# Optimization experiments

Measured on AMD Instinct MI355X. Metric: run time of the kernel, lower is better.

The kernel has to match this reference:

```python
import jax, jax.numpy as jnp
import numpy as np

N_NODES = 50000
N_EDGES = 800000
N_GRAPHS = 2000
F = 256          # node feature dim == hidden_dim (required by stacked convs)
HID = 256
L = 4
FP = 1034
BN_EPS = 1e-5


def setup_inputs() -> dict:
    key = jax.random.key(0)
    ks = jax.random.split(key, 20)
    s = 0.05
    x = jax.random.normal(ks[0], (N_NODES, F), dtype=jnp.float32)
    edge_index = jax.random.randint(ks[1], (2, N_EDGES), 0, N_NODES, dtype=jnp.int64)
    edge_attr = jax.random.normal(ks[2], (N_EDGES, 1), dtype=jnp.float32)
    fingerprint = jax.random.uniform(ks[3], (N_GRAPHS, FP), dtype=jnp.float32)
    batch = jnp.sort(jax.random.randint(ks[4], (N_NODES,), 0, N_GRAPHS, dtype=jnp.int64))
    # stacked per-layer conv params: message linear [(F+1)->HID], update linear [HID->HID]
    lin_w = jax.random.normal(ks[5], (L, F + 1, HID), dtype=jnp.float32) * s
    lin_b = jax.random.normal(ks[6], (L, HID), dtype=jnp.float32) * s
    upd_w = jax.random.normal(ks[7], (L, HID, HID), dtype=jnp.float32) * s
    upd_b = jax.random.normal(ks[8], (L, HID), dtype=jnp.float32) * s
    # gated-attention pooling gate_nn: Linear(HID,HID) -> tanh -> Linear(HID,1)
    g1_w = jax.random.normal(ks[9], (HID, HID), dtype=jnp.float32) * s
    g1_b = jax.random.normal(ks[10], (HID,), dtype=jnp.float32) * s
    g2_w = jax.random.normal(ks[11], (HID, 1), dtype=jnp.float32) * s
    g2_b = jax.random.normal(ks[12], (1,), dtype=jnp.float32) * s
    fc1_w = jax.random.normal(ks[13], (HID + FP, HID), dtype=jnp.float32) * s
    fc1_b = jax.random.normal(ks[14], (HID,), dtype=jnp.float32) * s
    bn_gamma = jnp.ones((HID,), dtype=jnp.float32)
    bn_beta = jnp.zeros((HID,), dtype=jnp.float32)
    fc2_w = jax.random.normal(ks[15], (HID, 1), dtype=jnp.float32) * s
    fc2_b = jax.random.normal(ks[16], (1,), dtype=jnp.float32) * s
    return dict(x=x, edge_index=edge_index, edge_attr=edge_attr,
                fingerprint=fingerprint, batch=batch,
                lin_w=lin_w, lin_b=lin_b, upd_w=upd_w, upd_b=upd_b,
                g1_w=g1_w, g1_b=g1_b, g2_w=g2_w, g2_b=g2_b,
                fc1_w=fc1_w, fc1_b=fc1_b, bn_gamma=bn_gamma, bn_beta=bn_beta,
                fc2_w=fc2_w, fc2_b=fc2_b)


def reference(x, edge_index, edge_attr, fingerprint, batch,
              lin_w, lin_b, upd_w, upd_b,
              g1_w, g1_b, g2_w, g2_b,
              fc1_w, fc1_b, bn_gamma, bn_beta, fc2_w, fc2_b):
    n = x.shape[0]
    b = fingerprint.shape[0]
    loop = jnp.arange(n, dtype=edge_index.dtype)
    src = jnp.concatenate([edge_index[0], loop])   # x_j = source nodes (PyG default)
    dst = jnp.concatenate([edge_index[1], loop])   # aggregate at target
    ea = jnp.concatenate([edge_attr, jnp.zeros((n, edge_attr.shape[1]), edge_attr.dtype)], axis=0)
    for l in range(L):
        wn, we = lin_w[l, :F], lin_w[l, F:]        # split concat([x_j, edge_attr]) @ W
        msg = jax.nn.relu(x[src] @ wn + ea @ we + lin_b[l])          # [E+n, HID]
        aggr = jax.ops.segment_sum(msg, dst, num_segments=n)          # scatter-add
        x = jax.nn.relu(aggr @ upd_w[l] + upd_b[l])
    # gated attention pooling
    gate = jax.nn.sigmoid(jnp.tanh(x @ g1_w + g1_b) @ g2_w + g2_b)    # [n, 1]
    pooled = jax.ops.segment_sum(x * gate, batch, num_segments=b)     # [b, HID]
    h = jnp.concatenate([pooled, fingerprint], axis=1) @ fc1_w + fc1_b
    # BatchNorm1d (training mode: biased batch stats)
    mu = jnp.mean(h, axis=0)
    var = jnp.mean((h - mu) ** 2, axis=0)
    h = (h - mu) * jax.lax.rsqrt(var + BN_EPS) * bn_gamma + bn_beta
    h = jax.nn.relu(h)  # dropout is identity in eval mode
    return (h @ fc2_w + fc2_b).squeeze(-1)        # [b]
```

## Files before the change

### kernel.cpp

```cpp
#include <hip/hip_runtime.h>
#include <math.h>

#define HIDF 256
#define FPDIM 1034
#define MPAD 50048
#define FCM 2048
#define FCK 1344

typedef _Float16 f16x8 __attribute__((ext_vector_type(8)));
typedef _Float16 f16x4 __attribute__((ext_vector_type(4)));
typedef float f32x4 __attribute__((ext_vector_type(4)));

__device__ __forceinline__ float relu_f(float v) { return fmaxf(v, 0.f); }

__global__ __launch_bounds__(256) void convxh_k(
    const float* __restrict__ x, _Float16* __restrict__ xh, int n)
{
    int i = blockIdx.x * 256 + threadIdx.x;
    int row = i >> 6;
    if (row >= MPAD) return;
    f16x4 o;
    if (row < n) {
        float4 v = ((const float4*)x)[i];
        o[0] = (_Float16)v.x; o[1] = (_Float16)v.y;
        o[2] = (_Float16)v.z; o[3] = (_Float16)v.w;
    } else {
        o[0] = o[1] = o[2] = o[3] = (_Float16)0.f;
    }
    ((f16x4*)xh)[i] = o;
}

__global__ __launch_bounds__(256) void convw_k(
    const float* __restrict__ w, _Float16* __restrict__ whi,
    _Float16* __restrict__ wlo)
{
    int i = blockIdx.x * 256 + threadIdx.x;
    int nn = i >> 8, kk = i & 255;
    float v = w[kk * 256 + nn];
    _Float16 h = (_Float16)v;
    _Float16 l = (_Float16)(v - (float)h);
    whi[i] = h;
    wlo[i] = l;
}

__global__ __launch_bounds__(256) void convfc1a_k(
    const float* __restrict__ pooled, const float* __restrict__ fp,
    _Float16* __restrict__ ahi, _Float16* __restrict__ alo, int B)
{
    int i = blockIdx.x * 256 + threadIdx.x;
    if (i >= FCM * FCK) return;
    int row = i / FCK, col = i - row * FCK;
    float v = 0.f;
    if (row < B) {
        if (col < HIDF) v = pooled[(size_t)row * HIDF + col];
        else if (col < HIDF + FPDIM) v = fp[(size_t)row * FPDIM + (col - HIDF)];
    }
    _Float16 h = (_Float16)v;
    _Float16 l = (_Float16)(v - (float)h);
    ahi[i] = h;
    alo[i] = l;
}

__global__ __launch_bounds__(256) void convfc1w_k(
    const float* __restrict__ w, _Float16* __restrict__ whi,
    _Float16* __restrict__ wlo)
{
    int i = blockIdx.x * 256 + threadIdx.x;
    if (i >= HIDF * FCK) return;
    int nn = i / FCK, kk = i - nn * FCK;
    float v = (kk < HIDF + FPDIM) ? w[(size_t)kk * HIDF + nn] : 0.f;
    _Float16 h = (_Float16)v;
    _Float16 l = (_Float16)(v - (float)h);
    whi[i] = h;
    wlo[i] = l;
}

template <int ACT>
__global__ __launch_bounds__(256) void gemm_f16(
    const _Float16* __restrict__ A, const _Float16* __restrict__ Whi,
    const _Float16* __restrict__ Wlo, const float* __restrict__ bias,
    _Float16* __restrict__ C, int M, int N, int K)
{
    __shared__ _Float16 As[128 * 64];
    __shared__ _Float16 Bh[128 * 64];
    __shared__ _Float16 Bl[128 * 64];
    const int tid = threadIdx.x;
    const int wave = tid >> 6, lane = tid & 63;
    const int m0 = blockIdx.y * 128, n0 = blockIdx.x * 128;
    const int wr = wave >> 1, wc = wave & 1;

    f32x4 acc[4][4];
#pragma unroll
    for (int i = 0; i < 4; ++i)
#pragma unroll
        for (int j = 0; j < 4; ++j) acc[i][j] = (f32x4){0.f, 0.f, 0.f, 0.f};

    const int lrow = lane >> 3;
    const int lcol8 = (lane & 7) * 8;

    for (int k0 = 0; k0 < K; k0 += 64) {
#pragma unroll
        for (int i = 0; i < 4; ++i) {
            int iss = wave * 4 + i;
            int row = 8 * iss + lrow;
            const _Float16* ga = A   + (size_t)(m0 + row) * K + k0 + lcol8;
            const _Float16* gh = Whi + (size_t)(n0 + row) * K + k0 + lcol8;
            const _Float16* gl = Wlo + (size_t)(n0 + row) * K + k0 + lcol8;
            __builtin_amdgcn_global_load_lds(
                (const __attribute__((address_space(1))) void*)ga,
                (__attribute__((address_space(3))) void*)(As + iss * 512), 16, 0, 0);
            __builtin_amdgcn_global_load_lds(
                (const __attribute__((address_space(1))) void*)gh,
                (__attribute__((address_space(3))) void*)(Bh + iss * 512), 16, 0, 0);
            __builtin_amdgcn_global_load_lds(
                (const __attribute__((address_space(1))) void*)gl,
                (__attribute__((address_space(3))) void*)(Bl + iss * 512), 16, 0, 0);
        }
        __syncthreads();
#pragma unroll
        for (int kk = 0; kk < 2; ++kk) {
            const int kb = kk * 32 + (lane >> 4) * 8;
            f16x8 af[4], bh[4], bl[4];
#pragma unroll
            for (int mi = 0; mi < 4; ++mi)
                af[mi] = *(const f16x8*)&As[(wr * 64 + mi * 16 + (lane & 15)) * 64 + kb];
#pragma unroll
            for (int ni = 0; ni < 4; ++ni) {
                int r = (wc * 64 + ni * 16 + (lane & 15)) * 64 + kb;
                bh[ni] = *(const f16x8*)&Bh[r];
                bl[ni] = *(const f16x8*)&Bl[r];
            }
#pragma unroll
            for (int mi = 0; mi < 4; ++mi)
#pragma unroll
                for (int ni = 0; ni < 4; ++ni) {
                    acc[mi][ni] = __builtin_amdgcn_mfma_f32_16x16x32_f16(
                        af[mi], bh[ni], acc[mi][ni], 0, 0, 0);
                    acc[mi][ni] = __builtin_amdgcn_mfma_f32_16x16x32_f16(
                        af[mi], bl[ni], acc[mi][ni], 0, 0, 0);
                }
        }
        __syncthreads();
    }

    const int crow0 = m0 + wr * 64 + (lane >> 4) * 4;
    const int ccol0 = n0 + wc * 64 + (lane & 15);
#pragma unroll
    for (int mi = 0; mi < 4; ++mi) {
#pragma unroll
        for (int ni = 0; ni < 4; ++ni) {
            int col = ccol0 + ni * 16;
            float bv = bias ? bias[col] : 0.f;
#pragma unroll
            for (int r = 0; r < 4; ++r) {
                int row = crow0 + mi * 16 + r;
                float v = acc[mi][ni][r] + bv;
                if (ACT == 1) v = relu_f(v);
                else if (ACT == 2) v = tanhf(v);
                C[(size_t)row * N + col] = (_Float16)v;
            }
        }
    }
}

__global__ __launch_bounds__(256) void gemm_fc1(
    const _Float16* __restrict__ Ahi, const _Float16* __restrict__ Alo,
    const _Float16* __restrict__ Whi, const _Float16* __restrict__ Wlo,
    const float* __restrict__ bias, float* __restrict__ C,
    int Mv, int N, int K)
{
    __shared__ _Float16 Ah[128 * 64];
    __shared__ _Float16 Al[128 * 64];
    __shared__ _Float16 Bh[128 * 64];
    __shared__ _Float16 Bl[128 * 64];
    const int tid = threadIdx.x;
    const int wave = tid >> 6, lane = tid & 63;
    const int m0 = blockIdx.y * 128, n0 = blockIdx.x * 128;
    const int wr = wave >> 1, wc = wave & 1;

    f32x4 acc[4][4];
#pragma unroll
    for (int i = 0; i < 4; ++i)
#pragma unroll
        for (int j = 0; j < 4; ++j) acc[i][j] = (f32x4){0.f, 0.f, 0.f, 0.f};

    const int lrow = lane >> 3;
    const int lcol8 = (lane & 7) * 8;

    for (int k0 = 0; k0 < K; k0 += 64) {
#pragma unroll
        for (int i = 0; i < 4; ++i) {
            int iss = wave * 4 + i;
            int row = 8 * iss + lrow;
            const _Float16* gah = Ahi + (size_t)(m0 + row) * K + k0 + lcol8;
            const _Float16* gal = Alo + (size_t)(m0 + row) * K + k0 + lcol8;
            const _Float16* gbh = Whi + (size_t)(n0 + row) * K + k0 + lcol8;
            const _Float16* gbl = Wlo + (size_t)(n0 + row) * K + k0 + lcol8;
            __builtin_amdgcn_global_load_lds(
                (const __attribute__((address_space(1))) void*)gah,
                (__attribute__((address_space(3))) void*)(Ah + iss * 512), 16, 0, 0);
            __builtin_amdgcn_global_load_lds(
                (const __attribute__((address_space(1))) void*)gal,
                (__attribute__((address_space(3))) void*)(Al + iss * 512), 16, 0, 0);
            __builtin_amdgcn_global_load_lds(
                (const __attribute__((address_space(1))) void*)gbh,
                (__attribute__((address_space(3))) void*)(Bh + iss * 512), 16, 0, 0);
            __builtin_amdgcn_global_load_lds(
                (const __attribute__((address_space(1))) void*)gbl,
                (__attribute__((address_space(3))) void*)(Bl + iss * 512), 16, 0, 0);
        }
        __syncthreads();
#pragma unroll
        for (int kk = 0; kk < 2; ++kk) {
            const int kb = kk * 32 + (lane >> 4) * 8;
            f16x8 ah[4], al[4], bh[4], bl[4];
#pragma unroll
            for (int mi = 0; mi < 4; ++mi) {
                int r = (wr * 64 + mi * 16 + (lane & 15)) * 64 + kb;
                ah[mi] = *(const f16x8*)&Ah[r];
                al[mi] = *(const f16x8*)&Al[r];
            }
#pragma unroll
            for (int ni = 0; ni < 4; ++ni) {
                int r = (wc * 64 + ni * 16 + (lane & 15)) * 64 + kb;
                bh[ni] = *(const f16x8*)&Bh[r];
                bl[ni] = *(const f16x8*)&Bl[r];
            }
#pragma unroll
            for (int mi = 0; mi < 4; ++mi)
#pragma unroll
                for (int ni = 0; ni < 4; ++ni) {
                    acc[mi][ni] = __builtin_amdgcn_mfma_f32_16x16x32_f16(
                        ah[mi], bh[ni], acc[mi][ni], 0, 0, 0);
                    acc[mi][ni] = __builtin_amdgcn_mfma_f32_16x16x32_f16(
                        ah[mi], bl[ni], acc[mi][ni], 0, 0, 0);
                    acc[mi][ni] = __builtin_amdgcn_mfma_f32_16x16x32_f16(
                        al[mi], bh[ni], acc[mi][ni], 0, 0, 0);
                }
        }
        __syncthreads();
    }

    const int crow0 = m0 + wr * 64 + (lane >> 4) * 4;
    const int ccol0 = n0 + wc * 64 + (lane & 15);
#pragma unroll
    for (int mi = 0; mi < 4; ++mi) {
#pragma unroll
        for (int ni = 0; ni < 4; ++ni) {
            int col = ccol0 + ni * 16;
            float bv = bias[col];
#pragma unroll
            for (int r = 0; r < 4; ++r) {
                int row = crow0 + mi * 16 + r;
                if (row < Mv)
                    C[(size_t)row * N + col] = acc[mi][ni][r] + bv;
            }
        }
    }
}

__global__ void count_k(const int* __restrict__ dst, int* __restrict__ cnt, int E)
{
    int e = blockIdx.x * blockDim.x + threadIdx.x;
    if (e < E) atomicAdd(&cnt[dst[e]], 1);
}

__global__ __launch_bounds__(256) void scan1_k(
    const int* __restrict__ cnt, int* __restrict__ offs,
    int* __restrict__ bsum, int n)
{
    __shared__ int sh[256];
    int t = threadIdx.x, idx = blockIdx.x * 256 + t;
    int v = (idx < n) ? cnt[idx] : 0;
    sh[t] = v;
    __syncthreads();
    for (int o = 1; o < 256; o <<= 1) {
        int a = (t >= o) ? sh[t - o] : 0;
        __syncthreads();
        sh[t] += a;
        __syncthreads();
    }
    if (idx < n) offs[idx] = sh[t] - v;
    if (t == 255) bsum[blockIdx.x] = sh[255];
}

__global__ __launch_bounds__(256) void scan2_k(int* __restrict__ bsum, int nb)
{
    __shared__ int sh[256];
    int t = threadIdx.x;
    int v = (t < nb) ? bsum[t] : 0;
    sh[t] = v;
    __syncthreads();
    for (int o = 1; o < 256; o <<= 1) {
        int a = (t >= o) ? sh[t - o] : 0;
        __syncthreads();
        sh[t] += a;
        __syncthreads();
    }
    if (t < nb) bsum[t] = sh[t] - v;
}

__global__ __launch_bounds__(256) void scan3_k(
    int* __restrict__ offs, const int* __restrict__ bsum,
    int* __restrict__ cursor, int n, int E)
{
    int idx = blockIdx.x * 256 + threadIdx.x;
    if (idx < n) {
        int o = offs[idx] + bsum[blockIdx.x];
        offs[idx] = o;
        cursor[idx] = o;
    }
    if (idx == 0) offs[n] = E;
}

__global__ void scatter_k(const int* __restrict__ dst, const int* __restrict__ src,
                          const float* __restrict__ ea, int* __restrict__ cursor,
                          int* __restrict__ srcS, float* __restrict__ eaS, int E)
{
    int e = blockIdx.x * blockDim.x + threadIdx.x;
    if (e < E) {
        int p = atomicAdd(&cursor[dst[e]], 1);
        srcS[p] = src[e];
        eaS[p] = ea[e];
    }
}

__global__ void start_k(const int* __restrict__ batch, int* __restrict__ start,
                        int n, int B)
{
    int g = blockIdx.x * blockDim.x + threadIdx.x;
    if (g > B) return;
    int lo = 0, hi = n;
    while (lo < hi) {
        int mid = (lo + hi) >> 1;
        if (batch[mid] < g) lo = mid + 1; else hi = mid;
    }
    start[g] = lo;
}

__global__ __launch_bounds__(256) void aggregate_k(
    const _Float16* __restrict__ xw, const float* __restrict__ we,
    const int* __restrict__ srcS, const float* __restrict__ eaS,
    const int* __restrict__ offs, _Float16* __restrict__ out, int n)
{
    int w = (blockIdx.x * blockDim.x + threadIdx.x) >> 6;
    if (w >= n) return;
    int lane = threadIdx.x & 63;
    int f = lane << 2;
    float4 we4 = *(const float4*)(we + f);
    f16x4 xs = *(const f16x4*)(xw + (size_t)w * HIDF + f);
    float4 acc;
    acc.x = relu_f((float)xs[0]);
    acc.y = relu_f((float)xs[1]);
    acc.z = relu_f((float)xs[2]);
    acc.w = relu_f((float)xs[3]);
    int e0 = offs[w], e1 = offs[w + 1];
    int ii = e0;
    for (; ii + 8 <= e1; ii += 8) {
        int s[8]; float a[8]; f16x4 v[8];
#pragma unroll
        for (int j = 0; j < 8; ++j) { s[j] = srcS[ii + j]; a[j] = eaS[ii + j]; }
#pragma unroll
        for (int j = 0; j < 8; ++j)
            v[j] = *(const f16x4*)(xw + (size_t)s[j] * HIDF + f);
#pragma unroll
        for (int j = 0; j < 8; ++j) {
            acc.x += relu_f(fmaf(a[j], we4.x, (float)v[j][0]));
            acc.y += relu_f(fmaf(a[j], we4.y, (float)v[j][1]));
            acc.z += relu_f(fmaf(a[j], we4.z, (float)v[j][2]));
            acc.w += relu_f(fmaf(a[j], we4.w, (float)v[j][3]));
        }
    }
    if (ii + 4 <= e1) {
        int s[4]; float a[4]; f16x4 v[4];
#pragma unroll
        for (int j = 0; j < 4; ++j) { s[j] = srcS[ii + j]; a[j] = eaS[ii + j]; }
#pragma unroll
        for (int j = 0; j < 4; ++j)
            v[j] = *(const f16x4*)(xw + (size_t)s[j] * HIDF + f);
#pragma unroll
        for (int j = 0; j < 4; ++j) {
            acc.x += relu_f(fmaf(a[j], we4.x, (float)v[j][0]));
            acc.y += relu_f(fmaf(a[j], we4.y, (float)v[j][1]));
            acc.z += relu_f(fmaf(a[j], we4.z, (float)v[j][2]));
            acc.w += relu_f(fmaf(a[j], we4.w, (float)v[j][3]));
        }
        ii += 4;
    }
    for (; ii < e1; ++ii) {
        int s0 = srcS[ii];
        float a0 = eaS[ii];
        f16x4 v0 = *(const f16x4*)(xw + (size_t)s0 * HIDF + f);
        acc.x += relu_f(fmaf(a0, we4.x, (float)v0[0]));
        acc.y += relu_f(fmaf(a0, we4.y, (float)v0[1]));
        acc.z += relu_f(fmaf(a0, we4.z, (float)v0[2]));
        acc.w += relu_f(fmaf(a0, we4.w, (float)v0[3]));
    }
    f16x4 o;
    o[0] = (_Float16)acc.x; o[1] = (_Float16)acc.y;
    o[2] = (_Float16)acc.z; o[3] = (_Float16)acc.w;
    *(f16x4*)(out + (size_t)w * HIDF + f) = o;
}

__global__ __launch_bounds__(256) void gate_k(
    const _Float16* __restrict__ t, const float* __restrict__ g2w,
    const float* __restrict__ g2b, float* __restrict__ gate, int n)
{
    int w = (blockIdx.x * blockDim.x + threadIdx.x) >> 6;
    if (w >= n) return;
    int lane = threadIdx.x & 63;
    f16x4 tv = *(const f16x4*)(t + (size_t)w * HIDF + (lane << 2));
    float4 g = *(const float4*)(g2w + (lane << 2));
    float s = (float)tv[0] * g.x + (float)tv[1] * g.y
            + (float)tv[2] * g.z + (float)tv[3] * g.w;
    for (int o = 32; o; o >>= 1) s += __shfl_xor(s, o);
    if (lane == 0) gate[w] = 1.f / (1.f + expf(-(s + g2b[0])));
}

__global__ __launch_bounds__(256) void pool_k(
    const _Float16* __restrict__ x, const float* __restrict__ gate,
    const int* __restrict__ start, float* __restrict__ pooled, int B)
{
    int w = (blockIdx.x * blockDim.x + threadIdx.x) >> 6;
    if (w >= B) return;
    int lane = threadIdx.x & 63;
    int f = lane << 2;
    float4 acc = make_float4(0.f, 0.f, 0.f, 0.f);
    int i0 = start[w], i1 = start[w + 1];
    for (int i = i0; i < i1; ++i) {
        float gi = gate[i];
        f16x4 v = *(const f16x4*)(x + (size_t)i * HIDF + f);
        acc.x = fmaf(gi, (float)v[0], acc.x);
        acc.y = fmaf(gi, (float)v[1], acc.y);
        acc.z = fmaf(gi, (float)v[2], acc.z);
        acc.w = fmaf(gi, (float)v[3], acc.w);
    }
    *(float4*)(pooled + (size_t)w * HIDF + f) = acc;
}

__global__ __launch_bounds__(256) void bnstats_k(
    const float* __restrict__ h, float* __restrict__ mu,
    float* __restrict__ rs, int B)
{
    int j = blockIdx.x;
    int tid = threadIdx.x;
    float s = 0.f, s2 = 0.f;
    for (int g = tid; g < B; g += 256) {
        float v = h[(size_t)g * HIDF + j];
        s += v;
        s2 = fmaf(v, v, s2);
    }
    __shared__ float sh[256], sh2[256];
    sh[tid] = s; sh2[tid] = s2;
    __syncthreads();
    for (int o = 128; o; o >>= 1) {
        if (tid < o) { sh[tid] += sh[tid + o]; sh2[tid] += sh2[tid + o]; }
        __syncthreads();
    }
    if (tid == 0) {
        float m = sh[0] / (float)B;
        float var = sh2[0] / (float)B - m * m;
        if (var < 0.f) var = 0.f;
        mu[j] = m;
        rs[j] = rsqrtf(var + 1e-5f);
    }
}

__global__ __launch_bounds__(256) void final_k(
    const float* __restrict__ h, const float* __restrict__ mu,
    const float* __restrict__ rs, const float* __restrict__ gamma,
    const float* __restrict__ beta, const float* __restrict__ w2,
    const float* __restrict__ b2, float* __restrict__ out, int B)
{
    int g = blockIdx.x;
    int j = threadIdx.x;
    float v = h[(size_t)g * HIDF + j];
    v = (v - mu[j]) * rs[j] * gamma[j] + beta[j];
    v = relu_f(v);
    float term = v * w2[j];
    __shared__ float sh[256];
    sh[j] = term;
    __syncthreads();
    for (int o = 128; o; o >>= 1) {
        if (j < o) sh[j] += sh[j + o];
        __syncthreads();
    }
    if (j == 0) out[g] = sh[0] + b2[0];
}

extern "C" void kernel_launch(void* const* d_in, const int* in_sizes, int n_in,
                              void* d_out, int out_size, void* d_ws, size_t ws_size,
                              hipStream_t stream)
{
    const float* x      = (const float*)d_in[0];
    const int*   ei     = (const int*)d_in[1];
    const float* ea     = (const float*)d_in[2];
    const float* fp     = (const float*)d_in[3];
    const int*   batch  = (const int*)d_in[4];
    const float* lin_w  = (const float*)d_in[5];
    const float* lin_b  = (const float*)d_in[6];
    const float* upd_w  = (const float*)d_in[7];
    const float* upd_b  = (const float*)d_in[8];
    const float* g1w    = (const float*)d_in[9];
    const float* g1b    = (const float*)d_in[10];
    const float* g2w    = (const float*)d_in[11];
    const float* g2b    = (const float*)d_in[12];
    const float* fc1w   = (const float*)d_in[13];
    const float* fc1b   = (const float*)d_in[14];
    const float* gamma  = (const float*)d_in[15];
    const float* beta   = (const float*)d_in[16];
    const float* fc2w   = (const float*)d_in[17];
    const float* fc2b   = (const float*)d_in[18];
    float* out = (float*)d_out;

    const int n = in_sizes[0] / HIDF;
    const int E = in_sizes[1] / 2;
    const int B = in_sizes[3] / FPDIM;
    const int L = in_sizes[5] / (257 * 256);
    const int* srcArr = ei;
    const int* dstArr = ei + E;
    const int nb = (n + 255) / 256;

    char* w = (char*)d_ws;
    _Float16* xh   = (_Float16*)w;  w += (size_t)MPAD * HIDF * 2;
    _Float16* bufA = (_Float16*)w;  w += (size_t)MPAD * HIDF * 2;
    _Float16* bufB = (_Float16*)w;  w += (size_t)MPAD * HIDF * 2;
    _Float16* whi = (_Float16*)w;  w += (size_t)9 * 65536 * 2;
    _Float16* wlo = (_Float16*)w;  w += (size_t)9 * 65536 * 2;
    _Float16* fahi = (_Float16*)w; w += (size_t)FCM * FCK * 2;
    _Float16* falo = (_Float16*)w; w += (size_t)FCM * FCK * 2;
    _Float16* fwhi = (_Float16*)w; w += (size_t)HIDF * FCK * 2;
    _Float16* fwlo = (_Float16*)w; w += (size_t)HIDF * FCK * 2;
    int*   srcS   = (int*)w;    w += (size_t)E * 4;
    float* eaS    = (float*)w;  w += (size_t)E * 4;
    int*   offs   = (int*)w;    w += ((size_t)n + 4) * 4;
    int*   cursor = (int*)w;    w += ((size_t)n + 4) * 4;
    int*   cnt    = (int*)w;    w += (size_t)n * 4;
    int*   bsum   = (int*)w;    w += 256 * 4;
    int*   startA = (int*)w;    w += ((size_t)B + 4) * 4;
    float* gateA  = (float*)w;  w += (size_t)n * 4;
    float* pooled = (float*)w;  w += (size_t)B * HIDF * 4;
    float* h      = (float*)w;  w += (size_t)B * HIDF * 4;
    float* mu     = (float*)w;  w += 256 * 4;
    float* rs     = (float*)w;  w += 256 * 4;

    hipMemsetAsync(cnt, 0, (size_t)n * 4, stream);
    count_k<<<(E + 255) / 256, 256, 0, stream>>>(dstArr, cnt, E);
    scan1_k<<<nb, 256, 0, stream>>>(cnt, offs, bsum, n);
    scan2_k<<<1, 256, 0, stream>>>(bsum, nb);
    scan3_k<<<nb, 256, 0, stream>>>(offs, bsum, cursor, n, E);
    scatter_k<<<(E + 255) / 256, 256, 0, stream>>>(dstArr, srcArr, ea, cursor, srcS, eaS, E);
    start_k<<<(B + 256) / 256, 256, 0, stream>>>(batch, startA, n, B);

    convxh_k<<<(MPAD * 64 + 255) / 256, 256, 0, stream>>>(x, xh, n);
    for (int l = 0; l < L; ++l) {
        convw_k<<<256, 256, 0, stream>>>(lin_w + (size_t)l * 257 * 256,
                                         whi + (size_t)l * 65536, wlo + (size_t)l * 65536);
        convw_k<<<256, 256, 0, stream>>>(upd_w + (size_t)l * 65536,
                                         whi + (size_t)(4 + l) * 65536, wlo + (size_t)(4 + l) * 65536);
    }
    convw_k<<<256, 256, 0, stream>>>(g1w, whi + (size_t)8 * 65536, wlo + (size_t)8 * 65536);
    convfc1w_k<<<(HIDF * FCK + 255) / 256, 256, 0, stream>>>(fc1w, fwhi, fwlo);

    dim3 ggm(HIDF / 128, MPAD / 128);
    for (int l = 0; l < L; ++l) {
        const float* we = lin_w + (size_t)l * 257 * 256 + 256 * 256;
        const float* lb = lin_b + (size_t)l * 256;
        gemm_f16<0><<<ggm, 256, 0, stream>>>(xh, whi + (size_t)l * 65536,
                                             wlo + (size_t)l * 65536, lb,
                                             bufA, MPAD, HIDF, HIDF);
        aggregate_k<<<(n * 64 + 255) / 256, 256, 0, stream>>>(
            bufA, we, srcS, eaS, offs, bufB, n);
        gemm_f16<1><<<ggm, 256, 0, stream>>>(bufB, whi + (size_t)(4 + l) * 65536,
                                             wlo + (size_t)(4 + l) * 65536,
                                             upd_b + (size_t)l * 256, xh, MPAD, HIDF, HIDF);
    }

    gemm_f16<2><<<ggm, 256, 0, stream>>>(xh, whi + (size_t)8 * 65536,
                                         wlo + (size_t)8 * 65536, g1b,
                                         bufA, MPAD, HIDF, HIDF);
    gate_k<<<(n * 64 + 255) / 256, 256, 0, stream>>>(bufA, g2w, g2b, gateA, n);
    pool_k<<<(B * 64 + 255) / 256, 256, 0, stream>>>(xh, gateA, startA, pooled, B);

    convfc1a_k<<<(FCM * FCK + 255) / 256, 256, 0, stream>>>(pooled, fp, fahi, falo, B);
    dim3 ggf(HIDF / 128, FCM / 128);
    gemm_fc1<<<ggf, 256, 0, stream>>>(fahi, falo, fwhi, fwlo, fc1b, h, B, HIDF, FCK);
    bnstats_k<<<256, 256, 0, stream>>>(h, mu, rs, B);
    final_k<<<B, 256, 0, stream>>>(h, mu, rs, gamma, beta, fc2w, fc2b, out, B);
}
```

Baseline: 717.5 us.

## Pack edge src/attr into int2 and split wavefront halves across edges

The sorted edge source index and edge attribute are packed into a single int2 array, so each edge needs one 8-byte load instead of two separate loads. The aggregate kernel now has each half-wavefront process alternate edges with 16-byte f16x8 feature loads per lane. The two halves' partial sums are combined with a cross-lane shuffle before the store. This widens per-lane memory transactions and doubles the edges in flight per wave, at the cost of half the lanes idling on odd-degree tails and an extra reduction step.

```diff
diff --git a/kernel.cpp b/kernel.cpp
--- a/kernel.cpp
+++ b/kernel.cpp
@@ -315,13 +315,12 @@
 
 __global__ void scatter_k(const int* __restrict__ dst, const int* __restrict__ src,
                           const float* __restrict__ ea, int* __restrict__ cursor,
-                          int* __restrict__ srcS, float* __restrict__ eaS, int E)
+                          int2* __restrict__ esrc, int E)
 {
     int e = blockIdx.x * blockDim.x + threadIdx.x;
     if (e < E) {
         int p = atomicAdd(&cursor[dst[e]], 1);
-        srcS[p] = src[e];
-        eaS[p] = ea[e];
+        esrc[p] = make_int2(src[e], __float_as_int(ea[e]));
     }
 }
 
@@ -340,66 +339,72 @@
 
 __global__ __launch_bounds__(256) void aggregate_k(
     const _Float16* __restrict__ xw, const float* __restrict__ we,
-    const int* __restrict__ srcS, const float* __restrict__ eaS,
-    const int* __restrict__ offs, _Float16* __restrict__ out, int n)
+    const int2* __restrict__ esrc, const int* __restrict__ offs,
+    _Float16* __restrict__ out, int n)
 {
     int w = (blockIdx.x * blockDim.x + threadIdx.x) >> 6;
     if (w >= n) return;
-    int lane = threadIdx.x & 63;
-    int f = lane << 2;
-    float4 we4 = *(const float4*)(we + f);
-    f16x4 xs = *(const f16x4*)(xw + (size_t)w * HIDF + f);
-    float4 acc;
-    acc.x = relu_f((float)xs[0]);
-    acc.y = relu_f((float)xs[1]);
-    acc.z = relu_f((float)xs[2]);
-    acc.w = relu_f((float)xs[3]);
-    int e0 = offs[w], e1 = offs[w + 1];
-    int ii = e0;
-    for (; ii + 8 <= e1; ii += 8) {
-        int s[8]; float a[8]; f16x4 v[8];
-#pragma unroll
-        for (int j = 0; j < 8; ++j) { s[j] = srcS[ii + j]; a[j] = eaS[ii + j]; }
+    const int lane = threadIdx.x & 63;
+    const int half = lane >> 5;
+    const int f8 = (lane & 31) << 3;
+
+    float we8[8];
+    *(float4*)&we8[0] = *(const float4*)(we + f8);
+    *(float4*)&we8[4] = *(const float4*)(we + f8 + 4);
+
+    f16x8 xs = *(const f16x8*)(xw + (size_t)w * HIDF + f8);
+    float acc[8];
+#pragma unroll
+    for (int j = 0; j < 8; ++j)
+        acc[j] = (half == 0) ? relu_f((float)xs[j]) : 0.f;
+
+    const int e0 = offs[w], e1 = offs[w + 1];
+    const int cntE = e1 - e0;
+    const int fullPairs = cntE >> 1;
+
+    int t = 0;
+    for (; t + 4 <= fullPairs; t += 4) {
+        int2 p[4]; f16x8 v[4];
+#pragma unroll
+        for (int q = 0; q < 4; ++q) p[q] = esrc[e0 + 2 * (t + q) + half];
+#pragma unroll
+        for (int q = 0; q < 4; ++q)
+            v[q] = *(const f16x8*)(xw + (size_t)p[q].x * HIDF + f8);
+#pragma unroll
+        for (int q = 0; q < 4; ++q) {
+            float a = __int_as_float(p[q].y);
+#pragma unroll
+            for (int j = 0; j < 8; ++j)
+                acc[j] += relu_f(fmaf(a, we8[j], (float)v[q][j]));
+        }
+    }
+    for (; t < fullPairs; ++t) {
+        int2 p = esrc[e0 + 2 * t + half];
+        f16x8 v = *(const f16x8*)(xw + (size_t)p.x * HIDF + f8);
+        float a = __int_as_float(p.y);
 #pragma unroll
         for (int j = 0; j < 8; ++j)
-            v[j] = *(const f16x4*)(xw + (size_t)s[j] * HIDF + f);
-#pragma unroll
-        for (int j = 0; j < 8; ++j) {
-            acc.x += relu_f(fmaf(a[j], we4.x, (float)v[j][0]));
-            acc.y += relu_f(fmaf(a[j], we4.y, (float)v[j][1]));
-            acc.z += relu_f(fmaf(a[j], we4.z, (float)v[j][2]));
-            acc.w += relu_f(fmaf(a[j], we4.w, (float)v[j][3]));
-        }
-    }
-    if (ii + 4 <= e1) {
-        int s[4]; float a[4]; f16x4 v[4];
-#pragma unroll
-        for (int j = 0; j < 4; ++j) { s[j] = srcS[ii + j]; a[j] = eaS[ii + j]; }
-#pragma unroll
-        for (int j = 0; j < 4; ++j)
-            v[j] = *(const f16x4*)(xw + (size_t)s[j] * HIDF + f);
-#pragma unroll
-        for (int j = 0; j < 4; ++j) {
-            acc.x += relu_f(fmaf(a[j], we4.x, (float)v[j][0]));
-            acc.y += relu_f(fmaf(a[j], we4.y, (float)v[j][1]));
-            acc.z += relu_f(fmaf(a[j], we4.z, (float)v[j][2]));
-            acc.w += relu_f(fmaf(a[j], we4.w, (float)v[j][3]));
-        }
-        ii += 4;
-    }
-    for (; ii < e1; ++ii) {
-        int s0 = srcS[ii];
-        float a0 = eaS[ii];
-        f16x4 v0 = *(const f16x4*)(xw + (size_t)s0 * HIDF + f);
-        acc.x += relu_f(fmaf(a0, we4.x, (float)v0[0]));
-        acc.y += relu_f(fmaf(a0, we4.y, (float)v0[1]));
-        acc.z += relu_f(fmaf(a0, we4.z, (float)v0[2]));
-        acc.w += relu_f(fmaf(a0, we4.w, (float)v0[3]));
-    }
-    f16x4 o;
-    o[0] = (_Float16)acc.x; o[1] = (_Float16)acc.y;
-    o[2] = (_Float16)acc.z; o[3] = (_Float16)acc.w;
-    *(f16x4*)(out + (size_t)w * HIDF + f) = o;
+            acc[j] += relu_f(fmaf(a, we8[j], (float)v[j]));
+    }
+    if ((cntE & 1) && half == 0) {
+        int2 p = esrc[e1 - 1];
+        f16x8 v = *(const f16x8*)(xw + (size_t)p.x * HIDF + f8);
+        float a = __int_as_float(p.y);
+#pragma unroll
+        for (int j = 0; j < 8; ++j)
+            acc[j] += relu_f(fmaf(a, we8[j], (float)v[j]));
+    }
+
+#pragma unroll
+    for (int j = 0; j < 8; ++j)
+        acc[j] += __shfl_xor(acc[j], 32);
+
+    if (half == 0) {
+        f16x8 o;
+#pragma unroll
+        for (int j = 0; j < 8; ++j) o[j] = (_Float16)acc[j];
+        *(f16x8*)(out + (size_t)w * HIDF + f8) = o;
+    }
 }
 
 __global__ __launch_bounds__(256) void gate_k(
@@ -531,8 +536,7 @@
     _Float16* falo = (_Float16*)w; w += (size_t)FCM * FCK * 2;
     _Float16* fwhi = (_Float16*)w; w += (size_t)HIDF * FCK * 2;
     _Float16* fwlo = (_Float16*)w; w += (size_t)HIDF * FCK * 2;
-    int*   srcS   = (int*)w;    w += (size_t)E * 4;
-    float* eaS    = (float*)w;  w += (size_t)E * 4;
+    int2*  esrc   = (int2*)w;   w += (size_t)E * 8;
     int*   offs   = (int*)w;    w += ((size_t)n + 4) * 4;
     int*   cursor = (int*)w;    w += ((size_t)n + 4) * 4;
     int*   cnt    = (int*)w;    w += (size_t)n * 4;
@@ -549,7 +553,7 @@
     scan1_k<<<nb, 256, 0, stream>>>(cnt, offs, bsum, n);
     scan2_k<<<1, 256, 0, stream>>>(bsum, nb);
     scan3_k<<<nb, 256, 0, stream>>>(offs, bsum, cursor, n, E);
-    scatter_k<<<(E + 255) / 256, 256, 0, stream>>>(dstArr, srcArr, ea, cursor, srcS, eaS, E);
+    scatter_k<<<(E + 255) / 256, 256, 0, stream>>>(dstArr, srcArr, ea, cursor, esrc, E);
     start_k<<<(B + 256) / 256, 256, 0, stream>>>(batch, startA, n, B);
 
     convxh_k<<<(MPAD * 64 + 255) / 256, 256, 0, stream>>>(x, xh, n);
@@ -570,7 +574,7 @@
                                              wlo + (size_t)l * 65536, lb,
                                              bufA, MPAD, HIDF, HIDF);
         aggregate_k<<<(n * 64 + 255) / 256, 256, 0, stream>>>(
-            bufA, we, srcS, eaS, offs, bufB, n);
+            bufA, we, esrc, offs, bufB, n);
         gemm_f16<1><<<ggm, 256, 0, stream>>>(bufB, whi + (size_t)(4 + l) * 65536,
                                              wlo + (size_t)(4 + l) * 65536,
                                              upd_b + (size_t)l * 256, xh, MPAD, HIDF, HIDF);
```

New measurement: 714.0 us. Within noise of the previous version (-0.5%).
